# Kernel tuning notes

Hardware: AMD Instinct MI355X
Metric: run time of the kernel (lower is better)

The kernel has to match this reference:

```python
import jax, jax.numpy as jnp
import numpy as np

B, T, D_MODEL, HEAD = 8, 2048, 1024, 64
NEG = -1e9  # finite mask fill; exp underflows to 0 in softmax, avoids inf/NaN


def setup_inputs() -> dict:
    key = jax.random.key(0)
    k1, k2, k3, k4, k5 = jax.random.split(key, 5)
    x = jax.random.normal(k1, (B, T, D_MODEL), dtype=jnp.float32)
    valid_lens = jax.random.randint(k2, (B,), 0, T)
    # nn.Linear(d_model, head_size, bias=False): y = x @ W, W: (d_model, head_size)
    s = 0.02
    Wq = jax.random.normal(k3, (D_MODEL, HEAD), dtype=jnp.float32) * s
    Wk = jax.random.normal(k4, (D_MODEL, HEAD), dtype=jnp.float32) * s
    Wv = jax.random.normal(k5, (D_MODEL, HEAD), dtype=jnp.float32) * s
    return {"x": x, "Wq": Wq, "Wk": Wk, "Wv": Wv, "valid_lens": valid_lens}


def reference(x, Wq, Wk, Wv, valid_lens):
    # x: (B, T, D), projections -> (B, T, H)
    q = jnp.einsum("btd,dh->bth", x, Wq)
    k = jnp.einsum("btd,dh->bth", x, Wk)
    v = jnp.einsum("btd,dh->bth", x, Wv)
    scale = k.shape[-1] ** -0.5
    wei = jnp.einsum("bqh,bkh->bqk", q, k) * scale  # (B, T, T)

    t = jnp.arange(T)
    causal = t[None, :] <= t[:, None]                     # (T, T) lower-tri
    valid = t[None, :] < valid_lens[:, None]              # (B, T)
    mask = causal[None, :, :] & valid[:, :, None] & valid[:, None, :]  # (B, T, T)

    wei = jnp.where(mask, wei, NEG)
    attn = jax.nn.softmax(wei, axis=2)
    # rows with no valid key get all-masked scores -> original code zeros them out
    row_all_masked = ~jnp.any(mask, axis=2)               # (B, T)
    attn = jnp.where(row_all_masked[:, :, None], 0.0, attn)
    # dropout(p=0.0) == identity
    out = jnp.einsum("bqk,bkh->bqh", attn, v)             # (B, T, H)
    return out
```

## Files before the change

kernel.cpp:

```cpp
#include <hip/hip_runtime.h>
#include <hip/hip_bf16.h>
#include <stdint.h>

#define T_   2048
#define DM_  1024
#define HD_  64
#define NROW 16384
#define SPLIT 4
#define BM   32
#define BK   64

typedef __attribute__((ext_vector_type(8))) __bf16 bf16x8;
typedef __attribute__((ext_vector_type(4))) __bf16 bf16x4;
typedef __attribute__((ext_vector_type(4))) float  f32x4;

__global__ void wconv_k(const float* __restrict__ Wq, const float* __restrict__ Wk,
                        const float* __restrict__ Wv, __bf16* __restrict__ wfrag) {
    int tid  = blockIdx.x * 256 + threadIdx.x;
    int lane = tid & 63;
    int t    = (tid >> 6) % 12;
    int kc   = tid / (12 * 64);
    int c = lane & 15, g = lane >> 4;
    int n = t * 16 + c;
    const float* W = (n < 64) ? Wq : (n < 128) ? Wk : Wv;
    int col = n & 63;
    int k0  = kc * 32 + g * 8;
    __bf16* dst = wfrag + (size_t)tid * 8;
#pragma unroll
    for (int j = 0; j < 8; ++j) dst[j] = (__bf16)W[(k0 + j) * HD_ + col];
}

__global__ __launch_bounds__(256, 2) void proj_k(const float* __restrict__ x,
        const __bf16* __restrict__ wfrag, __bf16* __restrict__ Qb,
        __bf16* __restrict__ Kb, __bf16* __restrict__ Vt) {
    __shared__ __bf16 abuf[2][BM][72];
    __shared__ __bf16 bbuf[2][2][12][512];
    int tid  = threadIdx.x;
    int lane = tid & 63, wave = tid >> 6;
    int mh = wave >> 1, th = wave & 1;
    int c = lane & 15, g = lane >> 4;
    int row0 = blockIdx.x * BM;
    int ar = tid >> 3, a0 = (tid & 7) * 8;
    const float* xrow = x + (size_t)(row0 + ar) * DM_ + a0;

    f32x4 acc[6];
#pragma unroll
    for (int t = 0; t < 6; ++t) acc[t] = (f32x4)0.f;

    {
#pragma unroll
        for (int i = 0; i < 6; ++i) {
            int p = wave * 6 + i;
            int kh = p / 12, tt = p % 12;
            const __bf16* src = wfrag + ((size_t)kh * 12 + tt) * 512 + lane * 8;
            __builtin_amdgcn_global_load_lds(
                (const __attribute__((address_space(1))) void*)src,
                (__attribute__((address_space(3))) void*)&bbuf[0][kh][tt][0], 16, 0, 0);
        }
        f32x4 x0 = *(const f32x4*)(xrow);
        f32x4 x1 = *(const f32x4*)(xrow + 4);
        bf16x8 a;
#pragma unroll
        for (int j = 0; j < 4; ++j) { a[j] = (__bf16)x0[j]; a[4 + j] = (__bf16)x1[j]; }
        *(bf16x8*)&abuf[0][ar][a0] = a;
    }

    for (int kk = 0; kk < 16; ++kk) {
        int buf = kk & 1, nb = buf ^ 1;
        __syncthreads();
        f32x4 x0, x1;
        bool hn = (kk + 1) < 16;
        if (hn) {
            const float* xp = xrow + (kk + 1) * BK;
            x0 = *(const f32x4*)(xp);
            x1 = *(const f32x4*)(xp + 4);
#pragma unroll
            for (int i = 0; i < 6; ++i) {
                int p = wave * 6 + i;
                int kh = p / 12, tt = p % 12;
                const __bf16* src = wfrag + (((size_t)(kk + 1) * 2 + kh) * 12 + tt) * 512 + lane * 8;
                __builtin_amdgcn_global_load_lds(
                    (const __attribute__((address_space(1))) void*)src,
                    (__attribute__((address_space(3))) void*)&bbuf[nb][kh][tt][0], 16, 0, 0);
            }
        }
#pragma unroll
        for (int kh = 0; kh < 2; ++kh) {
            bf16x8 af = *(const bf16x8*)&abuf[buf][mh * 16 + c][kh * 32 + g * 8];
#pragma unroll
            for (int t = 0; t < 6; ++t) {
                bf16x8 bfh = *(const bf16x8*)&bbuf[buf][kh][th * 6 + t][lane * 8];
                acc[t] = __builtin_amdgcn_mfma_f32_16x16x32_bf16(af, bfh, acc[t], 0, 0, 0);
            }
        }
        if (hn) {
            bf16x8 a;
#pragma unroll
            for (int j = 0; j < 4; ++j) { a[j] = (__bf16)x0[j]; a[4 + j] = (__bf16)x1[j]; }
            *(bf16x8*)&abuf[nb][ar][a0] = a;
        }
    }

#pragma unroll
    for (int t = 0; t < 6; ++t) {
        int tg = th * 6 + t;
        int n  = tg * 16 + c;
#pragma unroll
        for (int r = 0; r < 4; ++r) {
            int grow = row0 + mh * 16 + g * 4 + r;
            float v  = acc[t][r];
            if (n < 64)       Qb[(size_t)grow * HD_ + n] = (__bf16)(v * 0.18033688f);
            else if (n < 128) Kb[(size_t)grow * HD_ + (n - 64)] = (__bf16)v;
            else              Vt[(size_t)(grow >> 11) * (HD_ * T_) + (size_t)(n - 128) * T_ + (grow & 2047)] = (__bf16)v;
        }
    }
}

__global__ __launch_bounds__(128, 2) void attn_k(const __bf16* __restrict__ Qb,
        const __bf16* __restrict__ Kb, const __bf16* __restrict__ Vt,
        float* __restrict__ Opart, float* __restrict__ ml) {
    int split = blockIdx.x >> 9;
    int bid2  = blockIdx.x & 511;
    int half = bid2 >> 8, idx = bid2 & 255;
    int b = idx >> 5, p = idx & 31;
    int qb = half ? (63 - p) : p;
    int wave = threadIdx.x >> 6, lane = threadIdx.x & 63;
    int c = lane & 15, g = lane >> 4;
    int qg   = qb * 32 + wave * 16 + c;
    int tile = b * 128 + qb * 2 + wave;
    int nd2  = (qb + 2) >> 1;
    float m = -1e30f, lsum = 0.f;
    if (split < nd2) {
        const __bf16* qp = Qb + (size_t)(b * T_ + qg) * HD_ + g * 8;
        bf16x8 qf0 = *(const bf16x8*)qp;
        bf16x8 qf1 = *(const bf16x8*)(qp + 32);
        const __bf16* Kbase = Kb + (size_t)b * T_ * HD_;
        const __bf16* Vbase = Vt + (size_t)b * HD_ * T_;
        f32x4 o0 = (f32x4)0.f, o1 = (f32x4)0.f, o2 = (f32x4)0.f, o3 = (f32x4)0.f;
        __shared__ __bf16 plds[2][16][72];
        __bf16 (*pl)[72] = plds[wave];
        for (int kt = split; kt < nd2; kt += SPLIT) {
            int kv0 = kt * 64;
            const __bf16* kp = Kbase + (size_t)(kv0 + c) * HD_ + g * 8;
            bf16x8 ka00 = *(const bf16x8*)(kp);
            bf16x8 ka01 = *(const bf16x8*)(kp + 32);
            bf16x8 ka10 = *(const bf16x8*)(kp + 16 * HD_);
            bf16x8 ka11 = *(const bf16x8*)(kp + 16 * HD_ + 32);
            bf16x8 kb00 = *(const bf16x8*)(kp + 32 * HD_);
            bf16x8 kb01 = *(const bf16x8*)(kp + 32 * HD_ + 32);
            bf16x8 kb10 = *(const bf16x8*)(kp + 48 * HD_);
            bf16x8 kb11 = *(const bf16x8*)(kp + 48 * HD_ + 32);
            const __bf16* vp = Vbase + (size_t)c * T_ + kv0 + g * 8;
            bf16x8 v0a = *(const bf16x8*)(vp);
            bf16x8 v1a = *(const bf16x8*)(vp + 16 * T_);
            bf16x8 v2a = *(const bf16x8*)(vp + 32 * T_);
            bf16x8 v3a = *(const bf16x8*)(vp + 48 * T_);
            bf16x8 v0b = *(const bf16x8*)(vp + 32);
            bf16x8 v1b = *(const bf16x8*)(vp + 16 * T_ + 32);
            bf16x8 v2b = *(const bf16x8*)(vp + 32 * T_ + 32);
            bf16x8 v3b = *(const bf16x8*)(vp + 48 * T_ + 32);
            f32x4 sa0 = (f32x4)0.f, sa1 = (f32x4)0.f, sb0 = (f32x4)0.f, sb1 = (f32x4)0.f;
            sa0 = __builtin_amdgcn_mfma_f32_16x16x32_bf16(ka00, qf0, sa0, 0, 0, 0);
            sa0 = __builtin_amdgcn_mfma_f32_16x16x32_bf16(ka01, qf1, sa0, 0, 0, 0);
            sa1 = __builtin_amdgcn_mfma_f32_16x16x32_bf16(ka10, qf0, sa1, 0, 0, 0);
            sa1 = __builtin_amdgcn_mfma_f32_16x16x32_bf16(ka11, qf1, sa1, 0, 0, 0);
            sb0 = __builtin_amdgcn_mfma_f32_16x16x32_bf16(kb00, qf0, sb0, 0, 0, 0);
            sb0 = __builtin_amdgcn_mfma_f32_16x16x32_bf16(kb01, qf1, sb0, 0, 0, 0);
            sb1 = __builtin_amdgcn_mfma_f32_16x16x32_bf16(kb10, qf0, sb1, 0, 0, 0);
            sb1 = __builtin_amdgcn_mfma_f32_16x16x32_bf16(kb11, qf1, sb1, 0, 0, 0);
            float s[16];
#pragma unroll
            for (int r = 0; r < 4; ++r) {
                s[r] = sa0[r]; s[4 + r] = sa1[r]; s[8 + r] = sb0[r]; s[12 + r] = sb1[r];
            }
            if (kt == nd2 - 1) {
#pragma unroll
                for (int i = 0; i < 16; ++i) {
                    int kv = kv0 + (i >> 2) * 16 + g * 4 + (i & 3);
                    if (kv > qg) s[i] = -1e30f;
                }
            }
            float m0 = fmaxf(fmaxf(s[0], s[1]), fmaxf(s[2], s[3]));
            float m1 = fmaxf(fmaxf(s[4], s[5]), fmaxf(s[6], s[7]));
            float m2 = fmaxf(fmaxf(s[8], s[9]), fmaxf(s[10], s[11]));
            float m3 = fmaxf(fmaxf(s[12], s[13]), fmaxf(s[14], s[15]));
            float tm = fmaxf(fmaxf(m0, m1), fmaxf(m2, m3));
            tm = fmaxf(tm, __shfl_xor(tm, 16));
            tm = fmaxf(tm, __shfl_xor(tm, 32));
            float mn = fmaxf(m, tm);
            float al = __builtin_amdgcn_exp2f(m - mn);
#pragma unroll
            for (int i = 0; i < 16; ++i) s[i] = __builtin_amdgcn_exp2f(s[i] - mn);
            float p0 = (s[0] + s[1]) + (s[2] + s[3]);
            float p1 = (s[4] + s[5]) + (s[6] + s[7]);
            float p2 = (s[8] + s[9]) + (s[10] + s[11]);
            float p3 = (s[12] + s[13]) + (s[14] + s[15]);
            float ps = (p0 + p1) + (p2 + p3);
            ps += __shfl_xor(ps, 16);
            ps += __shfl_xor(ps, 32);
            lsum = lsum * al + ps;
            m = mn;
            o0 *= al; o1 *= al; o2 *= al; o3 *= al;
#pragma unroll
            for (int mt = 0; mt < 4; ++mt) {
                bf16x4 pv;
#pragma unroll
                for (int r = 0; r < 4; ++r) pv[r] = (__bf16)s[mt * 4 + r];
                *(bf16x4*)&pl[c][mt * 16 + g * 4] = pv;
            }
            bf16x8 pf0 = *(const bf16x8*)&pl[c][g * 8];
            bf16x8 pf1 = *(const bf16x8*)&pl[c][32 + g * 8];
            o0 = __builtin_amdgcn_mfma_f32_16x16x32_bf16(v0a, pf0, o0, 0, 0, 0);
            o1 = __builtin_amdgcn_mfma_f32_16x16x32_bf16(v1a, pf0, o1, 0, 0, 0);
            o2 = __builtin_amdgcn_mfma_f32_16x16x32_bf16(v2a, pf0, o2, 0, 0, 0);
            o3 = __builtin_amdgcn_mfma_f32_16x16x32_bf16(v3a, pf0, o3, 0, 0, 0);
            o0 = __builtin_amdgcn_mfma_f32_16x16x32_bf16(v0b, pf1, o0, 0, 0, 0);
            o1 = __builtin_amdgcn_mfma_f32_16x16x32_bf16(v1b, pf1, o1, 0, 0, 0);
            o2 = __builtin_amdgcn_mfma_f32_16x16x32_bf16(v2b, pf1, o2, 0, 0, 0);
            o3 = __builtin_amdgcn_mfma_f32_16x16x32_bf16(v3b, pf1, o3, 0, 0, 0);
        }
        float* op = Opart + ((size_t)tile * SPLIT + split) * 1024 + c * 64 + g * 4;
        *(f32x4*)(op)      = o0;
        *(f32x4*)(op + 16) = o1;
        *(f32x4*)(op + 32) = o2;
        *(f32x4*)(op + 48) = o3;
    }
    if (g == 0) {
        float* mlp = ml + ((size_t)tile * SPLIT + split) * 32 + c * 2;
        mlp[0] = m; mlp[1] = lsum;
    }
}

__global__ __launch_bounds__(256) void comb_k(const float* __restrict__ Opart,
        const float* __restrict__ ml, const int* __restrict__ vlen,
        float* __restrict__ out) {
    int tile = blockIdx.x;
    int b  = tile >> 7;
    int q0 = (tile & 127) * 16;
    int q  = threadIdx.x >> 4;
    int d0 = (threadIdx.x & 15) * 4;
    int qg = q0 + q;
    const float* mlp = ml + (size_t)tile * SPLIT * 32 + q * 2;
    float mj[SPLIT], lj[SPLIT];
#pragma unroll
    for (int j = 0; j < SPLIT; ++j) { mj[j] = mlp[j * 32]; lj[j] = mlp[j * 32 + 1]; }
    float M = fmaxf(fmaxf(mj[0], mj[1]), fmaxf(mj[2], mj[3]));
    f32x4 acc = (f32x4)0.f;
    float L = 0.f;
#pragma unroll
    for (int j = 0; j < SPLIT; ++j) {
        if (lj[j] > 0.f) {
            float sc = __builtin_amdgcn_exp2f(mj[j] - M);
            L += lj[j] * sc;
            f32x4 ov = *(const f32x4*)(Opart + ((size_t)tile * SPLIT + j) * 1024 + q * 64 + d0);
            acc += ov * sc;
        }
    }
    float inv = (qg < vlen[b]) ? 1.f / L : 0.f;
    f32x4 r = acc * inv;
    *(f32x4*)(out + ((size_t)(b * T_) + qg) * HD_ + d0) = r;
}

extern "C" void kernel_launch(void* const* d_in, const int* in_sizes, int n_in,
                              void* d_out, int out_size, void* d_ws, size_t ws_size,
                              hipStream_t stream) {
    const float* x   = (const float*)d_in[0];
    const float* Wq  = (const float*)d_in[1];
    const float* Wk  = (const float*)d_in[2];
    const float* Wv  = (const float*)d_in[3];
    const int*   vln = (const int*)d_in[4];
    float* out = (float*)d_out;

    __bf16* Qb    = (__bf16*)d_ws;
    __bf16* Kb    = Qb + (size_t)NROW * HD_;
    __bf16* Vt    = Kb + (size_t)NROW * HD_;
    __bf16* wfrag = Vt + (size_t)NROW * HD_;
    float*  Opart = (float*)(wfrag + 24576 * 8);
    float*  mlbuf = Opart + (size_t)1024 * SPLIT * 1024;

    wconv_k<<<96, 256, 0, stream>>>(Wq, Wk, Wv, wfrag);
    proj_k <<<512, 256, 0, stream>>>(x, wfrag, Qb, Kb, Vt);
    attn_k <<<512 * SPLIT, 128, 0, stream>>>(Qb, Kb, Vt, Opart, mlbuf);
    comb_k <<<1024, 256, 0, stream>>>(Opart, mlbuf, vln, out);
}
```

Measured before the change: 152.0 us.

## Switch projection GEMM to 32x32x16 MFMA with six waves and defer row-sum reduction

The projection kernel now uses 32x32x16 bf16 MFMA tiles, with six waves per block, each owning a 32-column slice of the fused QKV output, instead of four waves issuing 16x16x32 MFMAs. The weight fragment layout and LDS staging are reorganized to match, so only the first 256 threads stage x. Separately, the attention kernel's per-iteration cross-lane shuffle reduction of the softmax row sum is moved after the loop. This is valid because the rescale factor is uniform across the lanes involved. The aim is fewer MFMA issues and shuffles per tile, at the cost of larger blocks and a different occupancy profile.

```diff
diff --git a/kernel.cpp b/kernel.cpp
--- a/kernel.cpp
+++ b/kernel.cpp
@@ -10,59 +10,59 @@
 #define BM   32
 #define BK   64
 
-typedef __attribute__((ext_vector_type(8))) __bf16 bf16x8;
-typedef __attribute__((ext_vector_type(4))) __bf16 bf16x4;
-typedef __attribute__((ext_vector_type(4))) float  f32x4;
+typedef __attribute__((ext_vector_type(8)))  __bf16 bf16x8;
+typedef __attribute__((ext_vector_type(4)))  __bf16 bf16x4;
+typedef __attribute__((ext_vector_type(4)))  float  f32x4;
+typedef __attribute__((ext_vector_type(16))) float  f32x16;
 
 __global__ void wconv_k(const float* __restrict__ Wq, const float* __restrict__ Wk,
                         const float* __restrict__ Wv, __bf16* __restrict__ wfrag) {
     int tid  = blockIdx.x * 256 + threadIdx.x;
     int lane = tid & 63;
-    int t    = (tid >> 6) % 12;
-    int kc   = tid / (12 * 64);
-    int c = lane & 15, g = lane >> 4;
-    int n = t * 16 + c;
+    int t    = (tid >> 6) % 6;
+    int kc   = tid / (6 * 64);
+    int n = t * 32 + (lane & 31);
     const float* W = (n < 64) ? Wq : (n < 128) ? Wk : Wv;
     int col = n & 63;
-    int k0  = kc * 32 + g * 8;
+    int k0  = kc * 16 + (lane >> 5) * 8;
     __bf16* dst = wfrag + (size_t)tid * 8;
 #pragma unroll
     for (int j = 0; j < 8; ++j) dst[j] = (__bf16)W[(k0 + j) * HD_ + col];
 }
 
-__global__ __launch_bounds__(256, 2) void proj_k(const float* __restrict__ x,
+__global__ __launch_bounds__(384, 3) void proj_k(const float* __restrict__ x,
         const __bf16* __restrict__ wfrag, __bf16* __restrict__ Qb,
         __bf16* __restrict__ Kb, __bf16* __restrict__ Vt) {
-    __shared__ __bf16 abuf[2][BM][72];
-    __shared__ __bf16 bbuf[2][2][12][512];
+    __shared__ __bf16 abuf[2][4][64][8];
+    __shared__ __bf16 bbuf[2][4][6][64][8];
     int tid  = threadIdx.x;
     int lane = tid & 63, wave = tid >> 6;
-    int mh = wave >> 1, th = wave & 1;
-    int c = lane & 15, g = lane >> 4;
     int row0 = blockIdx.x * BM;
-    int ar = tid >> 3, a0 = (tid & 7) * 8;
-    const float* xrow = x + (size_t)(row0 + ar) * DM_ + a0;
-
-    f32x4 acc[6];
-#pragma unroll
-    for (int t = 0; t < 6; ++t) acc[t] = (f32x4)0.f;
+    bool stager = tid < 256;
+    int srow = tid >> 3, sc8 = tid & 7;
+    int s_sub = sc8 >> 1, s_lane = srow + 32 * (sc8 & 1);
+    const float* xp0 = x + (size_t)(row0 + srow) * DM_ + sc8 * 8;
+
+    f32x16 acc = (f32x16)0.f;
 
     {
 #pragma unroll
-        for (int i = 0; i < 6; ++i) {
-            int p = wave * 6 + i;
-            int kh = p / 12, tt = p % 12;
-            const __bf16* src = wfrag + ((size_t)kh * 12 + tt) * 512 + lane * 8;
+        for (int i = 0; i < 4; ++i) {
+            int ch = wave * 4 + i;
+            int s = ch / 6, t = ch % 6;
+            const __bf16* src = wfrag + ((size_t)(0 * 4 + s) * 6 + t) * 512 + lane * 8;
             __builtin_amdgcn_global_load_lds(
                 (const __attribute__((address_space(1))) void*)src,
-                (__attribute__((address_space(3))) void*)&bbuf[0][kh][tt][0], 16, 0, 0);
-        }
-        f32x4 x0 = *(const f32x4*)(xrow);
-        f32x4 x1 = *(const f32x4*)(xrow + 4);
-        bf16x8 a;
-#pragma unroll
-        for (int j = 0; j < 4; ++j) { a[j] = (__bf16)x0[j]; a[4 + j] = (__bf16)x1[j]; }
-        *(bf16x8*)&abuf[0][ar][a0] = a;
+                (__attribute__((address_space(3))) void*)&bbuf[0][s][t][0][0], 16, 0, 0);
+        }
+        if (stager) {
+            f32x4 x0 = *(const f32x4*)(xp0);
+            f32x4 x1 = *(const f32x4*)(xp0 + 4);
+            bf16x8 a;
+#pragma unroll
+            for (int j = 0; j < 4; ++j) { a[j] = (__bf16)x0[j]; a[4 + j] = (__bf16)x1[j]; }
+            *(bf16x8*)&abuf[0][s_sub][s_lane][0] = a;
+        }
     }
 
     for (int kk = 0; kk < 16; ++kk) {
@@ -71,48 +71,43 @@
         f32x4 x0, x1;
         bool hn = (kk + 1) < 16;
         if (hn) {
-            const float* xp = xrow + (kk + 1) * BK;
-            x0 = *(const f32x4*)(xp);
-            x1 = *(const f32x4*)(xp + 4);
-#pragma unroll
-            for (int i = 0; i < 6; ++i) {
-                int p = wave * 6 + i;
-                int kh = p / 12, tt = p % 12;
-                const __bf16* src = wfrag + (((size_t)(kk + 1) * 2 + kh) * 12 + tt) * 512 + lane * 8;
+#pragma unroll
+            for (int i = 0; i < 4; ++i) {
+                int ch = wave * 4 + i;
+                int s = ch / 6, t = ch % 6;
+                const __bf16* src = wfrag + ((size_t)((kk + 1) * 4 + s) * 6 + t) * 512 + lane * 8;
                 __builtin_amdgcn_global_load_lds(
                     (const __attribute__((address_space(1))) void*)src,
-                    (__attribute__((address_space(3))) void*)&bbuf[nb][kh][tt][0], 16, 0, 0);
-            }
-        }
-#pragma unroll
-        for (int kh = 0; kh < 2; ++kh) {
-            bf16x8 af = *(const bf16x8*)&abuf[buf][mh * 16 + c][kh * 32 + g * 8];
-#pragma unroll
-            for (int t = 0; t < 6; ++t) {
-                bf16x8 bfh = *(const bf16x8*)&bbuf[buf][kh][th * 6 + t][lane * 8];
-                acc[t] = __builtin_amdgcn_mfma_f32_16x16x32_bf16(af, bfh, acc[t], 0, 0, 0);
-            }
-        }
-        if (hn) {
+                    (__attribute__((address_space(3))) void*)&bbuf[nb][s][t][0][0], 16, 0, 0);
+            }
+            if (stager) {
+                const float* xp = xp0 + (kk + 1) * BK;
+                x0 = *(const f32x4*)(xp);
+                x1 = *(const f32x4*)(xp + 4);
+            }
+        }
+#pragma unroll
+        for (int s = 0; s < 4; ++s) {
+            bf16x8 af = *(const bf16x8*)&abuf[buf][s][lane][0];
+            bf16x8 bfh = *(const bf16x8*)&bbuf[buf][s][wave][lane][0];
+            acc = __builtin_amdgcn_mfma_f32_32x32x16_bf16(af, bfh, acc, 0, 0, 0);
+        }
+        if (hn && stager) {
             bf16x8 a;
 #pragma unroll
             for (int j = 0; j < 4; ++j) { a[j] = (__bf16)x0[j]; a[4 + j] = (__bf16)x1[j]; }
-            *(bf16x8*)&abuf[nb][ar][a0] = a;
-        }
-    }
-
-#pragma unroll
-    for (int t = 0; t < 6; ++t) {
-        int tg = th * 6 + t;
-        int n  = tg * 16 + c;
-#pragma unroll
-        for (int r = 0; r < 4; ++r) {
-            int grow = row0 + mh * 16 + g * 4 + r;
-            float v  = acc[t][r];
-            if (n < 64)       Qb[(size_t)grow * HD_ + n] = (__bf16)(v * 0.18033688f);
-            else if (n < 128) Kb[(size_t)grow * HD_ + (n - 64)] = (__bf16)v;
-            else              Vt[(size_t)(grow >> 11) * (HD_ * T_) + (size_t)(n - 128) * T_ + (grow & 2047)] = (__bf16)v;
-        }
+            *(bf16x8*)&abuf[nb][s_sub][s_lane][0] = a;
+        }
+    }
+
+    int n = wave * 32 + (lane & 31);
+#pragma unroll
+    for (int r = 0; r < 16; ++r) {
+        int grow = row0 + (r & 3) + 8 * (r >> 2) + 4 * (lane >> 5);
+        float v  = acc[r];
+        if (n < 64)       Qb[(size_t)grow * HD_ + n] = (__bf16)(v * 0.18033688f);
+        else if (n < 128) Kb[(size_t)grow * HD_ + (n - 64)] = (__bf16)v;
+        else              Vt[(size_t)(grow >> 11) * (HD_ * T_) + (size_t)(n - 128) * T_ + (grow & 2047)] = (__bf16)v;
     }
 }
 
@@ -196,8 +191,6 @@
             float p2 = (s[8] + s[9]) + (s[10] + s[11]);
             float p3 = (s[12] + s[13]) + (s[14] + s[15]);
             float ps = (p0 + p1) + (p2 + p3);
-            ps += __shfl_xor(ps, 16);
-            ps += __shfl_xor(ps, 32);
             lsum = lsum * al + ps;
             m = mn;
             o0 *= al; o1 *= al; o2 *= al; o3 *= al;
@@ -225,6 +218,8 @@
         *(f32x4*)(op + 32) = o2;
         *(f32x4*)(op + 48) = o3;
     }
+    lsum += __shfl_xor(lsum, 16);
+    lsum += __shfl_xor(lsum, 32);
     if (g == 0) {
         float* mlp = ml + ((size_t)tile * SPLIT + split) * 32 + c * 2;
         mlp[0] = m; mlp[1] = lsum;
@@ -279,7 +274,7 @@
     float*  mlbuf = Opart + (size_t)1024 * SPLIT * 1024;
 
     wconv_k<<<96, 256, 0, stream>>>(Wq, Wk, Wv, wfrag);
-    proj_k <<<512, 256, 0, stream>>>(x, wfrag, Qb, Kb, Vt);
+    proj_k <<<512, 384, 0, stream>>>(x, wfrag, Qb, Kb, Vt);
     attn_k <<<512 * SPLIT, 128, 0, stream>>>(Qb, Kb, Vt, Opart, mlbuf);
     comb_k <<<1024, 256, 0, stream>>>(Opart, mlbuf, vln, out);
 }
```

Measured after the change: 162.8 us. 1.07x slower.
